# Performance work log

Hardware: AMD Instinct MI355X
Metric: run time of the kernel (lower is better)

Reference implementation:

```python
import jax, jax.numpy as jnp
import numpy as np

N_EDGE_TYPES = 25
EF = 2  # edge feature dim (excluding type)
HID = 10


def _edge_nn(et, ef, emb, wh, bh, wg, bg):
    # y = relu(emb[et] * (ef@Wh+bh) + (ef@Wg+bg)) -> [E, in*out]
    return jax.nn.relu(emb[et] * (ef @ wh + bh) + (ef @ wg + bg))


def _nnconv(x, et, ef, src, dst, emb, wh, bh, wg, bg, root, bias, in_c, out_c):
    n = x.shape[0]
    w = _edge_nn(et, ef, emb, wh, bh, wg, bg).reshape(-1, in_c, out_c)  # [E,in,out]
    msg = jnp.einsum('ei,eio->eo', x[src], w)                          # per-edge matmul
    s = jax.ops.segment_sum(msg, dst, num_segments=n)
    cnt = jax.ops.segment_sum(jnp.ones((src.shape[0],), x.dtype), dst, num_segments=n)
    agg = s / jnp.maximum(cnt, 1.0)[:, None]                           # scatter-mean
    return agg + x @ root + bias


def _make_params(key, in_c, out_c):
    ks = jax.random.split(key, 6)
    d = in_c * out_c
    s = 0.1
    return dict(
        emb=jax.random.normal(ks[0], (N_EDGE_TYPES, d), jnp.float32) * s,
        wh=jax.random.normal(ks[1], (EF, d), jnp.float32) * s,
        bh=jax.random.normal(ks[2], (d,), jnp.float32) * s,
        wg=jax.random.normal(ks[3], (EF, d), jnp.float32) * s,
        bg=jax.random.normal(ks[4], (d,), jnp.float32) * s,
        root=jax.random.normal(ks[5], (in_c, out_c), jnp.float32) * s,
        bias=jnp.zeros((out_c,), jnp.float32),
    )


def setup_inputs() -> dict:
    key = jax.random.key(0)
    ks = jax.random.split(key, 12)
    N, E, IN_C, OUT_C, B = 50000, 250000, 16, 16, 8
    inp = {
        'x': jax.random.normal(ks[0], (N, IN_C), jnp.float32),
        'edge_feat': jax.random.normal(ks[1], (E, EF), jnp.float32),
        'edge_type': jax.random.randint(ks[2], (E,), 0, N_EDGE_TYPES),
        'edge_src': jax.random.randint(ks[3], (E,), 0, N),
        'edge_dst': jax.random.randint(ks[4], (E,), 0, N),
        'cell_type': jax.random.randint(ks[5], (N,), 0, 3),
        'batch_ids': jnp.sort(jax.random.randint(ks[6], (N,), 0, B)),
        'batch_size': B,
    }
    for i, (ic, oc) in enumerate([(IN_C, HID), (HID, HID), (HID, OUT_C)], start=1):
        p = _make_params(ks[6 + i], ic, oc)
        for k, v in p.items():
            inp[f'{k}{i}'] = v
    return inp


def reference(x, edge_feat,
              emb1, wh1, bh1, wg1, bg1, root1, bias1,
              emb2, wh2, bh2, wg2, bg2, root2, bias2,
              emb3, wh3, bh3, wg3, bg3, root3, bias3,
              edge_type, edge_src, edge_dst, cell_type, batch_ids, batch_size):
    in_c, out_c = x.shape[1], root3.shape[1]
    h = _nnconv(x, edge_type, edge_feat, edge_src, edge_dst,
                emb1, wh1, bh1, wg1, bg1, root1, bias1, in_c, HID)
    h = jax.nn.relu(h)  # dropout is identity in eval mode
    h = _nnconv(h, edge_type, edge_feat, edge_src, edge_dst,
                emb2, wh2, bh2, wg2, bg2, root2, bias2, HID, HID)
    h = jax.nn.relu(h)
    h = _nnconv(h, edge_type, edge_feat, edge_src, edge_dst,
                emb3, wh3, bh3, wg3, bg3, root3, bias3, HID, out_c)
    h = jax.nn.relu(h)
    # scatter-mean pooling over nodes with cell_type==1, grouped by graph id
    gate = (cell_type == 1).astype(jnp.int32)
    idx = gate * (batch_ids.astype(jnp.int32) + 1)  # 0 = discarded bucket
    nseg = batch_size + 1
    s = jax.ops.segment_sum(h, idx, num_segments=nseg)
    cnt = jax.ops.segment_sum(jnp.ones((h.shape[0],), h.dtype), idx, num_segments=nseg)
    pooled = s / jnp.maximum(cnt, 1.0)[:, None]
    return pooled[1:batch_size + 1, :]  # [B, out_c]
```

## Files before the change

kernel.cpp:

```cpp
#include <hip/hip_runtime.h>
#include <stdint.h>

#define IN1 16
#define HIDC 10
#define OUT3 16
#define NTYPES 25
#define MAXB 8
#define HSTR 12

#define D1 (IN1 * HIDC)
#define D2 (HIDC * HIDC)
#define D3 (HIDC * OUT3)

__global__ __launch_bounds__(256) void zero2_kernel(int* __restrict__ a, int na,
                                                    int* __restrict__ b, int nb) {
  int i = blockIdx.x * blockDim.x + threadIdx.x;
  int s = gridDim.x * blockDim.x;
  for (int j = i; j < na; j += s) a[j] = 0;
  for (int j = i; j < nb; j += s) b[j] = 0;
}

__global__ __launch_bounds__(256) void hist_kernel(const int* __restrict__ edst,
                                                   int* __restrict__ deg,
                                                   int* __restrict__ pos, int E) {
  int e = blockIdx.x * blockDim.x + threadIdx.x;
  if (e < E) pos[e] = atomicAdd(&deg[edst[e]], 1);
}

__global__ __launch_bounds__(256) void scan_part_kernel(const int* __restrict__ deg,
                                                        int* __restrict__ row_ptr,
                                                        int* __restrict__ bsum, int N) {
  __shared__ int wsums[4];
  int tid = threadIdx.x, lane = tid & 63, wid = tid >> 6;
  int idx0 = (blockIdx.x * 256 + tid) * 4;
  int4 v = make_int4(0, 0, 0, 0);
  if (idx0 < N)     v.x = deg[idx0];
  if (idx0 + 1 < N) v.y = deg[idx0 + 1];
  if (idx0 + 2 < N) v.z = deg[idx0 + 2];
  if (idx0 + 3 < N) v.w = deg[idx0 + 3];
  int s = v.x + v.y + v.z + v.w;
  int x = s;
  #pragma unroll
  for (int off = 1; off < 64; off <<= 1) {
    int y = __shfl_up(x, off);
    if (lane >= off) x += y;
  }
  if (lane == 63) wsums[wid] = x;
  __syncthreads();
  int wpre = 0;
  #pragma unroll
  for (int w = 0; w < 4; ++w) if (w < wid) wpre += wsums[w];
  int excl = x - s + wpre;
  if (idx0 < N)     row_ptr[idx0]     = excl;
  if (idx0 + 1 < N) row_ptr[idx0 + 1] = excl + v.x;
  if (idx0 + 2 < N) row_ptr[idx0 + 2] = excl + v.x + v.y;
  if (idx0 + 3 < N) row_ptr[idx0 + 3] = excl + v.x + v.y + v.z;
  if (tid == 255) bsum[blockIdx.x] = excl + s;
}

__global__ __launch_bounds__(64) void scan_bsum_kernel(int* __restrict__ bsum,
                                                       int* __restrict__ row_ptr,
                                                       int G, int N) {
  int tid = threadIdx.x;
  int v = (tid < G) ? bsum[tid] : 0;
  int x = v;
  #pragma unroll
  for (int off = 1; off < 64; off <<= 1) {
    int y = __shfl_up(x, off);
    if (tid >= off) x += y;
  }
  if (tid < G) bsum[tid] = x - v;
  if (tid == 63) row_ptr[N] = x;
}

__global__ __launch_bounds__(256) void scan_add_kernel(int* __restrict__ row_ptr,
                                                       const int* __restrict__ bsum,
                                                       int N) {
  int i = blockIdx.x * blockDim.x + threadIdx.x;
  if (i < N) row_ptr[i] += bsum[i >> 10];
}

__global__ __launch_bounds__(256) void permute_kernel(
    const int* __restrict__ edst, const int* __restrict__ esrc,
    const int* __restrict__ et, const float2* __restrict__ ef,
    const int* __restrict__ row_ptr, const int* __restrict__ pos,
    int4* __restrict__ edges, int E) {
  int e = blockIdx.x * blockDim.x + threadIdx.x;
  if (e >= E) return;
  int d = edst[e];
  int idx = row_ptr[d] + pos[e];
  float2 f = ef[e];
  int4 r;
  r.x = esrc[e];
  r.y = et[e];
  r.z = __float_as_int(f.x);
  r.w = __float_as_int(f.y);
  edges[idx] = r;
}

__global__ __launch_bounds__(256) void prep_kernel(
    const float* __restrict__ emb1, const float* __restrict__ wh1,
    const float* __restrict__ bh1, const float* __restrict__ wg1,
    const float* __restrict__ bg1,
    const float* __restrict__ emb2, const float* __restrict__ wh2,
    const float* __restrict__ bh2, const float* __restrict__ wg2,
    const float* __restrict__ bg2,
    const float* __restrict__ emb3, const float* __restrict__ wh3,
    const float* __restrict__ bh3, const float* __restrict__ wg3,
    const float* __restrict__ bg3,
    float4* __restrict__ P1, float4* __restrict__ P2, float4* __restrict__ P3)
{
  int i = blockIdx.x * 256 + threadIdx.x;
  const float *emb, *wh, *bh, *wg, *bg;
  float4* P; int D, k;
  if (i < NTYPES * D1) {
    emb = emb1; wh = wh1; bh = bh1; wg = wg1; bg = bg1; P = P1; D = D1; k = i;
  } else if (i < NTYPES * (D1 + D2)) {
    emb = emb2; wh = wh2; bh = bh2; wg = wg2; bg = bg2; P = P2; D = D2;
    k = i - NTYPES * D1;
  } else if (i < NTYPES * (D1 + D2 + D3)) {
    emb = emb3; wh = wh3; bh = bh3; wg = wg3; bg = bg3; P = P3; D = D3;
    k = i - NTYPES * (D1 + D2);
  } else return;
  int j = k - (k / D) * D;
  float e = emb[k];
  float4 p;
  p.x = fmaf(e, wh[j],     wg[j]);
  p.y = fmaf(e, wh[D + j], wg[D + j]);
  p.z = fmaf(e, bh[j],     bg[j]);
  p.w = 0.f;
  P[k] = p;
}

template<int IN_C, int O, int XS, bool POOL, int BS>
__global__ __launch_bounds__(BS) void layer_kernel(
    const float* __restrict__ xin,
    const int4* __restrict__ edges,
    const int* __restrict__ row_ptr,
    const float4* __restrict__ Pg,
    const float* __restrict__ root,
    const float* __restrict__ bias,
    float* __restrict__ hout,
    const int* __restrict__ ctype, const int* __restrict__ bids,
    float* __restrict__ pcnt,
    int N, int B)
{
  constexpr int D = IN_C * O;
  constexpr int TSTR = D + 1;
  constexpr int NPB = BS / 16;
  __shared__ float4 s_P[NTYPES * TSTR];
  __shared__ float s_psum[POOL ? (MAXB * 16) : 1];
  __shared__ float s_pcnt[POOL ? MAXB : 1];

  int tid = threadIdx.x;
  for (int k = tid; k < NTYPES * D; k += BS) {
    int t = k / D, j = k - t * D;
    s_P[t * TSTR + j] = Pg[k];
  }
  if (POOL) {
    for (int i = tid; i < MAXB * 16; i += BS) s_psum[i] = 0.f;
    for (int i = tid; i < MAXB; i += BS) s_pcnt[i] = 0.f;
  }
  __syncthreads();

  int nl = tid >> 4;
  int o = tid & 15;
  int oc = (O == 16) ? o : ((o < O) ? o : 0);
  int n = blockIdx.x * NPB + nl;

  float acc = 0.f;
  int start = 0, end = 0;
  if (n < N) { start = row_ptr[n]; end = row_ptr[n + 1]; }
  for (int e = start; e < end; ++e) {
    int4 r = edges[e];
    float f0 = __int_as_float(r.z), f1 = __int_as_float(r.w);
    const float4* __restrict__ pb = s_P + r.y * TSTR + oc;
    const float* __restrict__ xr = xin + (size_t)r.x * XS;
    #pragma unroll
    for (int q = 0; q < IN_C / 4; ++q) {
      float4 xq = ((const float4*)xr)[q];
      float4 p0 = pb[(4 * q + 0) * O];
      float4 p1 = pb[(4 * q + 1) * O];
      float4 p2 = pb[(4 * q + 2) * O];
      float4 p3 = pb[(4 * q + 3) * O];
      acc = fmaf(xq.x, fmaxf(fmaf(f0, p0.x, fmaf(f1, p0.y, p0.z)), 0.f), acc);
      acc = fmaf(xq.y, fmaxf(fmaf(f0, p1.x, fmaf(f1, p1.y, p1.z)), 0.f), acc);
      acc = fmaf(xq.z, fmaxf(fmaf(f0, p2.x, fmaf(f1, p2.y, p2.z)), 0.f), acc);
      acc = fmaf(xq.w, fmaxf(fmaf(f0, p3.x, fmaf(f1, p3.y, p3.z)), 0.f), acc);
    }
    if constexpr (IN_C % 4 == 2) {
      float2 xq = ((const float2*)xr)[IN_C / 2 - 1];
      float4 p0 = pb[(IN_C - 2) * O];
      float4 p1 = pb[(IN_C - 1) * O];
      acc = fmaf(xq.x, fmaxf(fmaf(f0, p0.x, fmaf(f1, p0.y, p0.z)), 0.f), acc);
      acc = fmaf(xq.y, fmaxf(fmaf(f0, p1.x, fmaf(f1, p1.y, p1.z)), 0.f), acc);
    }
  }

  if (n < N && o < O) {
    float inv = 1.0f / fmaxf((float)(end - start), 1.0f);
    float v = fmaf(acc, inv, bias[o]);
    const float* __restrict__ xr = xin + (size_t)n * XS;
    #pragma unroll
    for (int i = 0; i < IN_C; ++i) v = fmaf(xr[i], root[i * O + o], v);
    v = fmaxf(v, 0.f);
    if (!POOL) {
      hout[(size_t)n * HSTR + o] = v;
    } else {
      if (ctype[n] == 1) {
        int b = bids[n];
        atomicAdd(&s_psum[b * 16 + o], v);
        if (o == 0) atomicAdd(&s_pcnt[b], 1.0f);
      }
    }
  }

  if (POOL) {
    __syncthreads();
    for (int i = tid; i < B * 16; i += BS) {
      float v = s_psum[i];
      if (v != 0.f) atomicAdd(&hout[i], v);
    }
    for (int i = tid; i < B; i += BS) {
      float c = s_pcnt[i];
      if (c != 0.f) atomicAdd(&pcnt[i], c);
    }
  }
}

__global__ __launch_bounds__(256) void finalize_kernel(
    const float* __restrict__ psum, const float* __restrict__ pcnt,
    float* __restrict__ out, int B) {
  int i = blockIdx.x * blockDim.x + threadIdx.x;
  if (i >= B * OUT3) return;
  int b = i / OUT3;
  out[i] = psum[i] / fmaxf(pcnt[b], 1.0f);
}

extern "C" void kernel_launch(void* const* d_in, const int* in_sizes, int n_in,
                              void* d_out, int out_size, void* d_ws, size_t ws_size,
                              hipStream_t stream)
{
  const float* x     = (const float*)d_in[0];
  const float* ef    = (const float*)d_in[1];
  const int*   et    = (const int*)d_in[2];
  const int*   esrc  = (const int*)d_in[3];
  const int*   edst  = (const int*)d_in[4];
  const int*   ctype = (const int*)d_in[5];
  const int*   bids  = (const int*)d_in[6];
  const float* emb1 = (const float*)d_in[8];
  const float* wh1  = (const float*)d_in[9];
  const float* bh1  = (const float*)d_in[10];
  const float* wg1  = (const float*)d_in[11];
  const float* bg1  = (const float*)d_in[12];
  const float* root1= (const float*)d_in[13];
  const float* bias1= (const float*)d_in[14];
  const float* emb2 = (const float*)d_in[15];
  const float* wh2  = (const float*)d_in[16];
  const float* bh2  = (const float*)d_in[17];
  const float* wg2  = (const float*)d_in[18];
  const float* bg2  = (const float*)d_in[19];
  const float* root2= (const float*)d_in[20];
  const float* bias2= (const float*)d_in[21];
  const float* emb3 = (const float*)d_in[22];
  const float* wh3  = (const float*)d_in[23];
  const float* bh3  = (const float*)d_in[24];
  const float* wg3  = (const float*)d_in[25];
  const float* bg3  = (const float*)d_in[26];
  const float* root3= (const float*)d_in[27];
  const float* bias3= (const float*)d_in[28];

  const int N = in_sizes[0] / IN1;
  const int E = in_sizes[2];
  const int B = out_size / OUT3;

  int4* edges   = (int4*)d_ws;
  int*  deg     = (int*)(edges + E);
  int*  pos     = deg + N;
  int*  row_ptr = pos + E;
  int*  bsum    = row_ptr + (N + 1);
  uintptr_t pp  = ((uintptr_t)(bsum + 64) + 15) & ~(uintptr_t)15;
  float4* P1    = (float4*)pp;
  float4* P2    = P1 + NTYPES * D1;
  float4* P3    = P2 + NTYPES * D2;
  float* h1     = (float*)(P3 + NTYPES * D3);
  float* h2     = h1 + (size_t)N * HSTR;
  float* psum   = h2 + (size_t)N * HSTR;
  float* pcnt   = psum + (size_t)B * 16;

  const int nChunk = (N + 1023) / 1024;
  const int nPrep  = NTYPES * (D1 + D2 + D3);

  zero2_kernel<<<128, 256, 0, stream>>>(deg, N, (int*)psum, B * 16 + B);
  prep_kernel<<<(nPrep + 255) / 256, 256, 0, stream>>>(
      emb1, wh1, bh1, wg1, bg1, emb2, wh2, bh2, wg2, bg2,
      emb3, wh3, bh3, wg3, bg3, P1, P2, P3);
  hist_kernel<<<(E + 255) / 256, 256, 0, stream>>>(edst, deg, pos, E);
  scan_part_kernel<<<nChunk, 256, 0, stream>>>(deg, row_ptr, bsum, N);
  scan_bsum_kernel<<<1, 64, 0, stream>>>(bsum, row_ptr, nChunk, N);
  scan_add_kernel<<<(N + 255) / 256, 256, 0, stream>>>(row_ptr, bsum, N);
  permute_kernel<<<(E + 255) / 256, 256, 0, stream>>>(
      edst, esrc, et, (const float2*)ef, row_ptr, pos, edges, E);

  const int g512 = (N + 31) / 32;
  layer_kernel<IN1, HIDC, IN1, false, 512><<<g512, 512, 0, stream>>>(
      x, edges, row_ptr, P1, root1, bias1,
      h1, nullptr, nullptr, nullptr, N, B);
  layer_kernel<HIDC, HIDC, HSTR, false, 512><<<g512, 512, 0, stream>>>(
      h1, edges, row_ptr, P2, root2, bias2,
      h2, nullptr, nullptr, nullptr, N, B);

  const int g1024 = (N + 63) / 64;
  layer_kernel<HIDC, OUT3, HSTR, true, 1024><<<g1024, 1024, 0, stream>>>(
      h2, edges, row_ptr, P3, root3, bias3,
      psum, ctype, bids, pcnt, N, B);

  finalize_kernel<<<1, 256, 0, stream>>>(psum, pcnt, (float*)d_out, B);
}
```

Before: 253.2 us.

## Fuse whole pipeline into one cooperative persistent kernel with grid syncs

Replaces the chain of about eleven kernel launches (zeroing, prep, histogram, three-stage scan, permute, three layers, finalize) with a single cooperative kernel that runs each phase in turn, separated by grid-wide barriers. Within each layer, waves take node tiles from an atomic work counter instead of using a static grid mapping. This is meant to remove launch overhead and the gaps between the many small kernels. In exchange the grid is limited to the number of co-resident blocks, grid.sync costs are added, and the fixed 256-CU assumption may underfill or overfill the device.

After: 717.5 us. +183.4%, slower.

```diff
diff --git a/kernel.cpp b/kernel.cpp
--- a/kernel.cpp
+++ b/kernel.cpp
@@ -1,5 +1,8 @@
 #include <hip/hip_runtime.h>
+#include <hip/hip_cooperative_groups.h>
 #include <stdint.h>
+
+namespace cg = cooperative_groups;
 
 #define IN1 16
 #define HIDC 10
@@ -11,6 +14,235 @@
 #define D1 (IN1 * HIDC)
 #define D2 (HIDC * HIDC)
 #define D3 (HIDC * OUT3)
+
+struct MArgs {
+  const float* x; const float2* ef;
+  const int *et, *esrc, *edst, *ctype, *bids;
+  const float *emb1,*wh1,*bh1,*wg1,*bg1,*root1,*bias1;
+  const float *emb2,*wh2,*bh2,*wg2,*bg2,*root2,*bias2;
+  const float *emb3,*wh3,*bh3,*wg3,*bg3,*root3,*bias3;
+  int4* edges; int *deg,*pos,*row_ptr,*bsum,*ctrs;
+  float4 *P1,*P2,*P3;
+  float *h1,*h2,*psum,*pcnt,*out;
+  int N,E,B;
+};
+
+template<int IN_C, int O, int XS, bool POOL>
+__device__ __forceinline__ void layer_phase(
+    const MArgs& a, const float* __restrict__ xin,
+    const float4* __restrict__ Pg,
+    const float* __restrict__ root, const float* __restrict__ bias,
+    float* __restrict__ hout, int* __restrict__ ctr,
+    float4* s_P, float* s_psum, float* s_pcnt)
+{
+  constexpr int D = IN_C * O;
+  constexpr int TSTR = D + 1;
+  const int tid = threadIdx.x;
+  for (int k = tid; k < NTYPES * D; k += 512) {
+    int t = k / D, j = k - t * D;
+    s_P[t * TSTR + j] = Pg[k];
+  }
+  if (POOL) {
+    for (int i = tid; i < MAXB * 16; i += 512) s_psum[i] = 0.f;
+    for (int i = tid; i < MAXB; i += 512) s_pcnt[i] = 0.f;
+  }
+  __syncthreads();
+
+  const int o = tid & 15;
+  const int sub = (tid >> 4) & 3;
+  const int oc = (O == 16) ? o : ((o < O) ? o : 0);
+  const int nT = (a.N + 3) >> 2;
+  const int nPop = (nT + 1) >> 1;
+
+  for (;;) {
+    int p = 0;
+    if ((tid & 63) == 0) p = atomicAdd(ctr, 1);
+    p = __shfl(p, 0);
+    if (p >= nPop) break;
+    #pragma unroll
+    for (int s2 = 0; s2 < 2; ++s2) {
+      int tile = p * 2 + s2;
+      if (tile >= nT) break;
+      int n = tile * 4 + sub;
+      float acc = 0.f;
+      int start = 0, end = 0;
+      if (n < a.N) { start = a.row_ptr[n]; end = a.row_ptr[n + 1]; }
+      for (int e = start; e < end; ++e) {
+        int4 r = a.edges[e];
+        float f0 = __int_as_float(r.z), f1 = __int_as_float(r.w);
+        const float4* __restrict__ pb = s_P + r.y * TSTR + oc;
+        const float* __restrict__ xr = xin + (size_t)r.x * XS;
+        #pragma unroll
+        for (int q = 0; q < IN_C / 4; ++q) {
+          float4 xq = ((const float4*)xr)[q];
+          float4 p0 = pb[(4 * q + 0) * O];
+          float4 p1 = pb[(4 * q + 1) * O];
+          float4 p2 = pb[(4 * q + 2) * O];
+          float4 p3 = pb[(4 * q + 3) * O];
+          acc = fmaf(xq.x, fmaxf(fmaf(f0, p0.x, fmaf(f1, p0.y, p0.z)), 0.f), acc);
+          acc = fmaf(xq.y, fmaxf(fmaf(f0, p1.x, fmaf(f1, p1.y, p1.z)), 0.f), acc);
+          acc = fmaf(xq.z, fmaxf(fmaf(f0, p2.x, fmaf(f1, p2.y, p2.z)), 0.f), acc);
+          acc = fmaf(xq.w, fmaxf(fmaf(f0, p3.x, fmaf(f1, p3.y, p3.z)), 0.f), acc);
+        }
+        if constexpr (IN_C % 4 == 2) {
+          float2 xq = ((const float2*)xr)[IN_C / 2 - 1];
+          float4 p0 = pb[(IN_C - 2) * O];
+          float4 p1 = pb[(IN_C - 1) * O];
+          acc = fmaf(xq.x, fmaxf(fmaf(f0, p0.x, fmaf(f1, p0.y, p0.z)), 0.f), acc);
+          acc = fmaf(xq.y, fmaxf(fmaf(f0, p1.x, fmaf(f1, p1.y, p1.z)), 0.f), acc);
+        }
+      }
+      if (n < a.N && o < O) {
+        float inv = 1.0f / fmaxf((float)(end - start), 1.0f);
+        float v = fmaf(acc, inv, bias[o]);
+        const float* __restrict__ xr = xin + (size_t)n * XS;
+        #pragma unroll
+        for (int i = 0; i < IN_C; ++i) v = fmaf(xr[i], root[i * O + o], v);
+        v = fmaxf(v, 0.f);
+        if (!POOL) {
+          hout[(size_t)n * HSTR + o] = v;
+        } else {
+          if (a.ctype[n] == 1) {
+            int b = a.bids[n];
+            atomicAdd(&s_psum[b * 16 + o], v);
+            if (o == 0) atomicAdd(&s_pcnt[b], 1.0f);
+          }
+        }
+      }
+    }
+  }
+
+  if (POOL) {
+    __syncthreads();
+    for (int i = tid; i < a.B * 16; i += 512) {
+      float v = s_psum[i];
+      if (v != 0.f) atomicAdd(&a.psum[i], v);
+    }
+    for (int i = tid; i < a.B; i += 512) {
+      float c = s_pcnt[i];
+      if (c != 0.f) atomicAdd(&a.pcnt[i], c);
+    }
+  }
+}
+
+__global__ __launch_bounds__(512) void mega_kernel(MArgs a)
+{
+  cg::grid_group grid = cg::this_grid();
+  __shared__ __align__(16) float4 s_P[NTYPES * (D1 + 1)];
+  __shared__ float s_psum[MAXB * 16];
+  __shared__ float s_pcnt[MAXB];
+  __shared__ int s_w[8];
+
+  const int tid = threadIdx.x;
+  const int gtid = blockIdx.x * 512 + tid;
+  const int gstr = gridDim.x * 512;
+
+  const int nPrep = NTYPES * (D1 + D2 + D3);
+  for (int i = gtid; i < nPrep; i += gstr) {
+    const float *emb, *wh, *bh, *wg, *bg; float4* P; int D, k;
+    if (i < NTYPES * D1) {
+      emb = a.emb1; wh = a.wh1; bh = a.bh1; wg = a.wg1; bg = a.bg1;
+      P = a.P1; D = D1; k = i;
+    } else if (i < NTYPES * (D1 + D2)) {
+      emb = a.emb2; wh = a.wh2; bh = a.bh2; wg = a.wg2; bg = a.bg2;
+      P = a.P2; D = D2; k = i - NTYPES * D1;
+    } else {
+      emb = a.emb3; wh = a.wh3; bh = a.bh3; wg = a.wg3; bg = a.bg3;
+      P = a.P3; D = D3; k = i - NTYPES * (D1 + D2);
+    }
+    int j = k - (k / D) * D;
+    float e = emb[k];
+    float4 p;
+    p.x = fmaf(e, wh[j],     wg[j]);
+    p.y = fmaf(e, wh[D + j], wg[D + j]);
+    p.z = fmaf(e, bh[j],     bg[j]);
+    p.w = 0.f;
+    P[k] = p;
+  }
+  for (int i = gtid; i < a.N; i += gstr) a.deg[i] = 0;
+  for (int i = gtid; i < a.B * 16; i += gstr) a.psum[i] = 0.f;
+  for (int i = gtid; i < a.B; i += gstr) a.pcnt[i] = 0.f;
+  if (gtid < 4) a.ctrs[gtid] = 0;
+  grid.sync();
+
+  for (int e = gtid; e < a.E; e += gstr) a.pos[e] = atomicAdd(&a.deg[a.edst[e]], 1);
+  grid.sync();
+
+  const int chunks = (a.N + 1023) >> 10;
+  if (blockIdx.x < chunks) {
+    int c = blockIdx.x;
+    int idx0 = (c << 10) + tid * 2;
+    int vx = (idx0 < a.N) ? a.deg[idx0] : 0;
+    int vy = (idx0 + 1 < a.N) ? a.deg[idx0 + 1] : 0;
+    int s = vx + vy;
+    int x = s;
+    int lane = tid & 63, wid = tid >> 6;
+    #pragma unroll
+    for (int off = 1; off < 64; off <<= 1) {
+      int y = __shfl_up(x, off);
+      if (lane >= off) x += y;
+    }
+    if (lane == 63) s_w[wid] = x;
+    __syncthreads();
+    if (tid < 8) {
+      int w = s_w[tid];
+      #pragma unroll
+      for (int off = 1; off < 8; off <<= 1) {
+        int y = __shfl_up(w, off);
+        if (tid >= off) w += y;
+      }
+      s_w[tid] = w;
+    }
+    __syncthreads();
+    int excl = x - s + ((wid > 0) ? s_w[wid - 1] : 0);
+    if (idx0 < a.N)     a.row_ptr[idx0]     = excl;
+    if (idx0 + 1 < a.N) a.row_ptr[idx0 + 1] = excl + vx;
+    if (tid == 511) a.bsum[c] = excl + s;
+  }
+  grid.sync();
+  if (blockIdx.x == 0 && tid < 64) {
+    int v = (tid < chunks) ? a.bsum[tid] : 0;
+    int x = v;
+    #pragma unroll
+    for (int off = 1; off < 64; off <<= 1) {
+      int y = __shfl_up(x, off);
+      if (tid >= off) x += y;
+    }
+    if (tid < chunks) a.bsum[tid] = x - v;
+    if (tid == 63) a.row_ptr[a.N] = x;
+  }
+  grid.sync();
+  for (int i = gtid; i < a.N; i += gstr) a.row_ptr[i] += a.bsum[i >> 10];
+  grid.sync();
+
+  for (int e = gtid; e < a.E; e += gstr) {
+    int d = a.edst[e];
+    int idx = a.row_ptr[d] + a.pos[e];
+    float2 f = a.ef[e];
+    int4 r;
+    r.x = a.esrc[e];
+    r.y = a.et[e];
+    r.z = __float_as_int(f.x);
+    r.w = __float_as_int(f.y);
+    a.edges[idx] = r;
+  }
+  grid.sync();
+
+  layer_phase<IN1, HIDC, IN1, false>(a, a.x, a.P1, a.root1, a.bias1,
+                                     a.h1, a.ctrs + 0, s_P, s_psum, s_pcnt);
+  grid.sync();
+  layer_phase<HIDC, HIDC, HSTR, false>(a, a.h1, a.P2, a.root2, a.bias2,
+                                       a.h2, a.ctrs + 1, s_P, s_psum, s_pcnt);
+  grid.sync();
+  layer_phase<HIDC, OUT3, HSTR, true>(a, a.h2, a.P3, a.root3, a.bias3,
+                                      a.psum, a.ctrs + 2, s_P, s_psum, s_pcnt);
+  grid.sync();
+
+  if (blockIdx.x == 0 && tid < a.B * OUT3) {
+    int b = tid / OUT3;
+    a.out[tid] = a.psum[tid] / fmaxf(a.pcnt[b], 1.0f);
+  }
+}
 
 __global__ __launch_bounds__(256) void zero2_kernel(int* __restrict__ a, int na,
                                                     int* __restrict__ b, int nb) {
@@ -134,16 +366,11 @@
 
 template<int IN_C, int O, int XS, bool POOL, int BS>
 __global__ __launch_bounds__(BS) void layer_kernel(
-    const float* __restrict__ xin,
-    const int4* __restrict__ edges,
-    const int* __restrict__ row_ptr,
-    const float4* __restrict__ Pg,
-    const float* __restrict__ root,
-    const float* __restrict__ bias,
-    float* __restrict__ hout,
-    const int* __restrict__ ctype, const int* __restrict__ bids,
-    float* __restrict__ pcnt,
-    int N, int B)
+    const float* __restrict__ xin, const int4* __restrict__ edges,
+    const int* __restrict__ row_ptr, const float4* __restrict__ Pg,
+    const float* __restrict__ root, const float* __restrict__ bias,
+    float* __restrict__ hout, const int* __restrict__ ctype,
+    const int* __restrict__ bids, float* __restrict__ pcnt, int N, int B)
 {
   constexpr int D = IN_C * O;
   constexpr int TSTR = D + 1;
@@ -279,7 +506,8 @@
   int*  pos     = deg + N;
   int*  row_ptr = pos + E;
   int*  bsum    = row_ptr + (N + 1);
-  uintptr_t pp  = ((uintptr_t)(bsum + 64) + 15) & ~(uintptr_t)15;
+  int*  ctrs    = bsum + 64;
+  uintptr_t pp  = ((uintptr_t)(ctrs + 4) + 15) & ~(uintptr_t)15;
   float4* P1    = (float4*)pp;
   float4* P2    = P1 + NTYPES * D1;
   float4* P3    = P2 + NTYPES * D2;
@@ -288,32 +516,62 @@
   float* psum   = h2 + (size_t)N * HSTR;
   float* pcnt   = psum + (size_t)B * 16;
 
-  const int nChunk = (N + 1023) / 1024;
-  const int nPrep  = NTYPES * (D1 + D2 + D3);
-
-  zero2_kernel<<<128, 256, 0, stream>>>(deg, N, (int*)psum, B * 16 + B);
-  prep_kernel<<<(nPrep + 255) / 256, 256, 0, stream>>>(
-      emb1, wh1, bh1, wg1, bg1, emb2, wh2, bh2, wg2, bg2,
-      emb3, wh3, bh3, wg3, bg3, P1, P2, P3);
-  hist_kernel<<<(E + 255) / 256, 256, 0, stream>>>(edst, deg, pos, E);
-  scan_part_kernel<<<nChunk, 256, 0, stream>>>(deg, row_ptr, bsum, N);
-  scan_bsum_kernel<<<1, 64, 0, stream>>>(bsum, row_ptr, nChunk, N);
-  scan_add_kernel<<<(N + 255) / 256, 256, 0, stream>>>(row_ptr, bsum, N);
-  permute_kernel<<<(E + 255) / 256, 256, 0, stream>>>(
-      edst, esrc, et, (const float2*)ef, row_ptr, pos, edges, E);
-
-  const int g512 = (N + 31) / 32;
-  layer_kernel<IN1, HIDC, IN1, false, 512><<<g512, 512, 0, stream>>>(
-      x, edges, row_ptr, P1, root1, bias1,
-      h1, nullptr, nullptr, nullptr, N, B);
-  layer_kernel<HIDC, HIDC, HSTR, false, 512><<<g512, 512, 0, stream>>>(
-      h1, edges, row_ptr, P2, root2, bias2,
-      h2, nullptr, nullptr, nullptr, N, B);
-
-  const int g1024 = (N + 63) / 64;
-  layer_kernel<HIDC, OUT3, HSTR, true, 1024><<<g1024, 1024, 0, stream>>>(
-      h2, edges, row_ptr, P3, root3, bias3,
-      psum, ctype, bids, pcnt, N, B);
-
-  finalize_kernel<<<1, 256, 0, stream>>>(psum, pcnt, (float*)d_out, B);
-}
+  static int coopBlocks = -2;
+  if (coopBlocks == -2) {
+    int nb = 0;
+    hipError_t qe = hipOccupancyMaxActiveBlocksPerMultiprocessor(
+        &nb, mega_kernel, 512, 0);
+    coopBlocks = (qe == hipSuccess && nb >= 1) ? nb * 256 : -1;
+  }
+
+  bool done = false;
+  if (coopBlocks > 0) {
+    MArgs ma;
+    ma.x = x; ma.ef = (const float2*)ef;
+    ma.et = et; ma.esrc = esrc; ma.edst = edst; ma.ctype = ctype; ma.bids = bids;
+    ma.emb1=emb1; ma.wh1=wh1; ma.bh1=bh1; ma.wg1=wg1; ma.bg1=bg1; ma.root1=root1; ma.bias1=bias1;
+    ma.emb2=emb2; ma.wh2=wh2; ma.bh2=bh2; ma.wg2=wg2; ma.bg2=bg2; ma.root2=root2; ma.bias2=bias2;
+    ma.emb3=emb3; ma.wh3=wh3; ma.bh3=bh3; ma.wg3=wg3; ma.bg3=bg3; ma.root3=root3; ma.bias3=bias3;
+    ma.edges = edges; ma.deg = deg; ma.pos = pos; ma.row_ptr = row_ptr;
+    ma.bsum = bsum; ma.ctrs = ctrs;
+    ma.P1 = P1; ma.P2 = P2; ma.P3 = P3;
+    ma.h1 = h1; ma.h2 = h2; ma.psum = psum; ma.pcnt = pcnt;
+    ma.out = (float*)d_out;
+    ma.N = N; ma.E = E; ma.B = B;
+    void* kargs[] = { &ma };
+    hipError_t le = hipLaunchCooperativeKernel(
+        (void*)mega_kernel, dim3(coopBlocks), dim3(512), kargs, 0, stream);
+    if (le == hipSuccess) done = true;
+  }
+
+  if (!done) {
+    const int nChunk = (N + 1023) / 1024;
+    const int nPrep  = NTYPES * (D1 + D2 + D3);
+
+    zero2_kernel<<<128, 256, 0, stream>>>(deg, N, (int*)psum, B * 16 + B);
+    prep_kernel<<<(nPrep + 255) / 256, 256, 0, stream>>>(
+        emb1, wh1, bh1, wg1, bg1, emb2, wh2, bh2, wg2, bg2,
+        emb3, wh3, bh3, wg3, bg3, P1, P2, P3);
+    hist_kernel<<<(E + 255) / 256, 256, 0, stream>>>(edst, deg, pos, E);
+    scan_part_kernel<<<nChunk, 256, 0, stream>>>(deg, row_ptr, bsum, N);
+    scan_bsum_kernel<<<1, 64, 0, stream>>>(bsum, row_ptr, nChunk, N);
+    scan_add_kernel<<<(N + 255) / 256, 256, 0, stream>>>(row_ptr, bsum, N);
+    permute_kernel<<<(E + 255) / 256, 256, 0, stream>>>(
+        edst, esrc, et, (const float2*)ef, row_ptr, pos, edges, E);
+
+    const int g512 = (N + 31) / 32;
+    layer_kernel<IN1, HIDC, IN1, false, 512><<<g512, 512, 0, stream>>>(
+        x, edges, row_ptr, P1, root1, bias1,
+        h1, nullptr, nullptr, nullptr, N, B);
+    layer_kernel<HIDC, HIDC, HSTR, false, 512><<<g512, 512, 0, stream>>>(
+        h1, edges, row_ptr, P2, root2, bias2,
+        h2, nullptr, nullptr, nullptr, N, B);
+
+    const int g1024 = (N + 63) / 64;
+    layer_kernel<HIDC, OUT3, HSTR, true, 1024><<<g1024, 1024, 0, stream>>>(
+        h2, edges, row_ptr, P3, root3, bias3,
+        psum, ctype, bids, pcnt, N, B);
+
+    finalize_kernel<<<1, 256, 0, stream>>>(psum, pcnt, (float*)d_out, B);
+  }
+}
```
